# Optimization experiments

Hardware: AMD Instinct MI355X
Metric: run time of the kernel (lower is better)

Reference implementation:

```python
import jax, jax.numpy as jnp
import numpy as np

H = 256        # hidden_size
MAX_LEN = 200  # position table has MAX_LEN+1 rows
B = 4096       # number of sessions


def setup_inputs() -> dict:
    rng = np.random.RandomState(0)
    # ragged session lengths in [10, 100)
    seq_len = rng.randint(10, 100, size=B).astype(np.int64)
    T = int(seq_len.sum())
    # reverse positions: len-1, ..., 1, 0 per session (as the torch code uses)
    reverse_pos = np.concatenate([np.arange(l - 1, -1, -1) for l in seq_len]).astype(np.int64)

    key = jax.random.key(0)
    ks = jax.random.split(key, 8)
    def lin(k, fin, fout):
        # torch Linear init ~ U(-1/sqrt(fin), 1/sqrt(fin)); store as [fin, fout]
        lim = 1.0 / np.sqrt(fin)
        kw, kb = jax.random.split(k)
        W = jax.random.uniform(kw, (fin, fout), jnp.float32, -lim, lim)
        b = jax.random.uniform(kb, (fout,), jnp.float32, -lim, lim)
        return W, b

    hidden = jax.random.normal(ks[0], (T, H), jnp.float32)
    pos_table = jax.random.normal(ks[1], (MAX_LEN + 1, H), jnp.float32)
    W_pos, b_pos = lin(ks[2], 2 * H, H)   # W_pos_inter
    W1, b1 = lin(ks[3], H, H)             # W_1_inter
    W2, b2 = lin(ks[4], H, H)             # W_2_inter
    qw, qb = lin(ks[5], H, 1)             # q_inter

    return {
        "hidden": hidden,
        "pos_table": pos_table,
        "W_pos": W_pos, "b_pos": b_pos,
        "W1": W1, "b1": b1,
        "W2": W2, "b2": b2,
        "qw": qw, "qb": qb,
        "seq_len": jnp.asarray(seq_len),
        "reverse_pos": jnp.asarray(reverse_pos),
    }


def reference(hidden, pos_table, W_pos, b_pos, W1, b1, W2, b2, qw, qb, seq_len, reverse_pos):
    T = hidden.shape[0]
    nb = seq_len.shape[0]
    # segment id per token (sessions are contiguous)
    seg = jnp.repeat(jnp.arange(nb), seq_len, total_repeat_length=T)  # [T]
    # per-session mean, gathered back per token (v_mean_repeat_concat)
    sess_mean = jax.ops.segment_sum(hidden, seg, num_segments=nb)
    sess_mean = sess_mean / seq_len[:, None].astype(hidden.dtype)
    v_mean = sess_mean[seg]                                           # [T, H]
    # position-augmented hidden: tanh(W_pos_inter([hidden; pos_emb]))
    pos_emb = pos_table[reverse_pos]                                  # [T, H]
    pos_hidden = jnp.tanh(jnp.concatenate([hidden, pos_emb], -1) @ W_pos + b_pos)
    # alpha = q_inter(sigmoid(W_1_inter(v_mean) + W_2_inter(pos_hidden)))
    gate = jax.nn.sigmoid(v_mean @ W1 + b1 + pos_hidden @ W2 + b2)
    alpha = gate @ qw + qb                                            # [T, 1]
    # per-session weighted sum of hidden
    h_s = jax.ops.segment_sum(alpha * hidden, seg, num_segments=nb)   # [B, H]
    return h_s
```

## Files before the change

kernel.cpp:

```cpp
#include <hip/hip_runtime.h>
#include <hip/hip_bf16.h>
#include <stdint.h>

#define HD 256
#define BM 64
#define APAD 8
#define ASTRIDE (HD + APAD)

typedef __bf16 bf16x8 __attribute__((ext_vector_type(8)));
typedef float f32x4 __attribute__((ext_vector_type(4)));
typedef unsigned short ushort8v __attribute__((ext_vector_type(8)));
typedef unsigned short us4 __attribute__((ext_vector_type(4)));

__device__ __forceinline__ unsigned short f2bf(float f) {
    unsigned int x = __float_as_uint(f);
    unsigned int r = (x + 0x7FFFu + ((x >> 16) & 1u)) >> 16;
    return (unsigned short)r;
}

__global__ void scan_kernel(const int* __restrict__ seq_len, int* __restrict__ offsets, int B) {
    __shared__ int sums[256];
    int tid = threadIdx.x;
    int per = (B + 255) / 256;
    int b0 = tid * per;
    int local[32];
    int tot = 0;
    for (int i = 0; i < per && i < 32; ++i) {
        int b = b0 + i;
        int v = (b < B) ? seq_len[b] : 0;
        local[i] = tot;
        tot += v;
    }
    sums[tid] = tot;
    __syncthreads();
    for (int off = 1; off < 256; off <<= 1) {
        int v = (tid >= off) ? sums[tid - off] : 0;
        __syncthreads();
        sums[tid] += v;
        __syncthreads();
    }
    int start = sums[tid] - tot;
    for (int i = 0; i < per && i < 32; ++i) {
        int b = b0 + i;
        if (b < B) offsets[b] = start + local[i];
    }
    if (tid == 255) offsets[B] = sums[255];
}

__global__ void mean_kernel(const float* __restrict__ hidden, const int* __restrict__ offsets,
                            unsigned short* __restrict__ mean_bf, unsigned short* __restrict__ hb,
                            int* __restrict__ seg) {
    int b = blockIdx.x;
    int s = offsets[b], e = offsets[b + 1];
    int tid = threadIdx.x;
    for (int t = s + tid; t < e; t += 256) seg[t] = b;
    int g = tid >> 6, c = tid & 63;
    float4 acc = {0.f, 0.f, 0.f, 0.f};
    for (int t = s + g; t < e; t += 4) {
        const float4 v = *reinterpret_cast<const float4*>(hidden + (size_t)t * HD + c * 4);
        acc.x += v.x; acc.y += v.y; acc.z += v.z; acc.w += v.w;
        if (hb) {
            us4 pk;
            pk[0] = f2bf(v.x); pk[1] = f2bf(v.y); pk[2] = f2bf(v.z); pk[3] = f2bf(v.w);
            *reinterpret_cast<us4*>(hb + (size_t)t * HD + c * 4) = pk;
        }
    }
    __shared__ float4 part[4][64];
    part[g][c] = acc;
    __syncthreads();
    if (g == 0) {
        float4 a0 = part[0][c], a1 = part[1][c], a2 = part[2][c], a3 = part[3][c];
        float inv = 1.0f / (float)(e - s);
        us4 pk;
        pk[0] = f2bf((a0.x + a1.x + a2.x + a3.x) * inv);
        pk[1] = f2bf((a0.y + a1.y + a2.y + a3.y) * inv);
        pk[2] = f2bf((a0.z + a1.z + a2.z + a3.z) * inv);
        pk[3] = f2bf((a0.w + a1.w + a2.w + a3.w) * inv);
        *reinterpret_cast<us4*>(mean_bf + (size_t)b * HD + c * 4) = pk;
    }
}

__global__ void transpose_kernel(const float* __restrict__ Wp, const float* __restrict__ W1,
                                 const float* __restrict__ W2,
                                 unsigned short* __restrict__ WphT, unsigned short* __restrict__ WpbT,
                                 unsigned short* __restrict__ W1T, unsigned short* __restrict__ W2T) {
    int n = blockIdx.x;
    int k = threadIdx.x;
    WphT[n * HD + k] = f2bf(Wp[k * HD + n]);
    WpbT[n * HD + k] = f2bf(Wp[(HD + k) * HD + n]);
    W1T[n * HD + k]  = f2bf(W1[k * HD + n]);
    W2T[n * HD + k]  = f2bf(W2[k * HD + n]);
}

__global__ __launch_bounds__(256) void small_gemm_kernel(
    const unsigned short* __restrict__ mean_bf, int Mu, int nbu,
    const float* __restrict__ pos_table, int Mp,
    const unsigned short* __restrict__ W1T, const unsigned short* __restrict__ WpbT,
    const float* __restrict__ b1, const float* __restrict__ b2, const float* __restrict__ bp,
    float* __restrict__ u, float* __restrict__ P2) {
    __shared__ __align__(16) unsigned short As[16][ASTRIDE];
    int tid = threadIdx.x;
    bool isU = (int)blockIdx.x < nbu;
    int m0 = isU ? blockIdx.x * 16 : (blockIdx.x - nbu) * 16;
    int M  = isU ? Mu : Mp;
    const unsigned short* BT = isU ? W1T : WpbT;
    float* out = isU ? u : P2;

    {
        int row = tid >> 4;
        int colg = (tid & 15) * 16;
        int m = m0 + row;
        if (isU) {
            ushort8v v0 = {0,0,0,0,0,0,0,0}, v1 = {0,0,0,0,0,0,0,0};
            if (m < M) {
                v0 = *reinterpret_cast<const ushort8v*>(mean_bf + (size_t)m * HD + colg);
                v1 = *reinterpret_cast<const ushort8v*>(mean_bf + (size_t)m * HD + colg + 8);
            }
            *reinterpret_cast<ushort8v*>(&As[row][colg])     = v0;
            *reinterpret_cast<ushort8v*>(&As[row][colg + 8]) = v1;
        } else {
            float4 f[4] = {{0,0,0,0},{0,0,0,0},{0,0,0,0},{0,0,0,0}};
            if (m < M) {
                const float4* p = reinterpret_cast<const float4*>(pos_table + (size_t)m * HD + colg);
                f[0] = p[0]; f[1] = p[1]; f[2] = p[2]; f[3] = p[3];
            }
            ushort8v v0, v1;
            v0[0]=f2bf(f[0].x); v0[1]=f2bf(f[0].y); v0[2]=f2bf(f[0].z); v0[3]=f2bf(f[0].w);
            v0[4]=f2bf(f[1].x); v0[5]=f2bf(f[1].y); v0[6]=f2bf(f[1].z); v0[7]=f2bf(f[1].w);
            v1[0]=f2bf(f[2].x); v1[1]=f2bf(f[2].y); v1[2]=f2bf(f[2].z); v1[3]=f2bf(f[2].w);
            v1[4]=f2bf(f[3].x); v1[5]=f2bf(f[3].y); v1[6]=f2bf(f[3].z); v1[7]=f2bf(f[3].w);
            *reinterpret_cast<ushort8v*>(&As[row][colg])     = v0;
            *reinterpret_cast<ushort8v*>(&As[row][colg + 8]) = v1;
        }
    }
    __syncthreads();

    int wave = tid >> 6, lane = tid & 63, quad = lane >> 4, cc = lane & 15;
    int nb = wave * 64;
    f32x4 acc4[4];
    for (int i = 0; i < 4; ++i) acc4[i] = (f32x4){0.f, 0.f, 0.f, 0.f};

    bf16x8 wfp[4];
    for (int nf = 0; nf < 4; ++nf)
        wfp[nf] = *reinterpret_cast<const bf16x8*>(BT + (size_t)(nb + nf * 16 + cc) * HD + quad * 8);
    for (int kc8 = 0; kc8 < 8; ++kc8) {
        int kc = kc8 * 32;
        bf16x8 wfc[4];
        for (int nf = 0; nf < 4; ++nf) wfc[nf] = wfp[nf];
        if (kc8 < 7)
            for (int nf = 0; nf < 4; ++nf)
                wfp[nf] = *reinterpret_cast<const bf16x8*>(BT + (size_t)(nb + nf * 16 + cc) * HD + kc + 32 + quad * 8);
        bf16x8 af = *reinterpret_cast<const bf16x8*>(&As[cc][kc + quad * 8]);
        for (int nf = 0; nf < 4; ++nf)
            acc4[nf] = __builtin_amdgcn_mfma_f32_16x16x32_bf16(af, wfc[nf], acc4[nf], 0, 0, 0);
    }
    for (int nf = 0; nf < 4; ++nf)
        for (int r = 0; r < 4; ++r) {
            int row = m0 + quad * 4 + r;
            int col = nb + nf * 16 + cc;
            if (row < M) {
                float bias = isU ? (b1[col] + b2[col]) : bp[col];
                out[(size_t)row * HD + col] = acc4[nf][r] + bias;
            }
        }
}

__global__ __launch_bounds__(256, 3) void main_kernel(
    const float* __restrict__ hidden, const unsigned short* __restrict__ hb, int T,
    const unsigned short* __restrict__ WphT,
    const unsigned short* __restrict__ W2T,
    const float* __restrict__ P2,
    const float* __restrict__ u,
    const float* __restrict__ qw, const float* __restrict__ qb,
    const int* __restrict__ rp, const int* __restrict__ seg,
    float* __restrict__ alpha) {
    __shared__ __align__(16) unsigned short Ah[BM][ASTRIDE];
    __shared__ int rp_s[BM];
    __shared__ int seg_s[BM];
    __shared__ float alpha_s[BM];

    int tid = threadIdx.x;
    int t0 = blockIdx.x * BM;
    int wave = tid >> 6, lane = tid & 63, quad = lane >> 4, cc = lane & 15;
    int mb = wave * 64;

    bf16x8 afp[4];
    for (int mf = 0; mf < 4; ++mf)
        afp[mf] = *reinterpret_cast<const bf16x8*>(WphT + (size_t)(mb + mf * 16 + cc) * HD + quad * 8);

    {
        int row = tid >> 2;
        int t = t0 + row;
        if (hb) {
            for (int i = 0; i < 8; ++i) {
                int cg = (tid & 3) * 8 + 32 * i;
                ushort8v v = {0,0,0,0,0,0,0,0};
                if (t < T) v = *reinterpret_cast<const ushort8v*>(hb + (size_t)t * HD + cg);
                *reinterpret_cast<ushort8v*>(&Ah[row][cg]) = v;
            }
        } else {
            for (int i = 0; i < 8; ++i) {
                int cg = (tid & 3) * 8 + 32 * i;
                float4 f0 = {0,0,0,0}, f1 = {0,0,0,0};
                if (t < T) {
                    const float4* p = reinterpret_cast<const float4*>(hidden + (size_t)t * HD + cg);
                    f0 = p[0]; f1 = p[1];
                }
                ushort8v pk;
                pk[0] = f2bf(f0.x); pk[1] = f2bf(f0.y); pk[2] = f2bf(f0.z); pk[3] = f2bf(f0.w);
                pk[4] = f2bf(f1.x); pk[5] = f2bf(f1.y); pk[6] = f2bf(f1.z); pk[7] = f2bf(f1.w);
                *reinterpret_cast<ushort8v*>(&Ah[row][cg]) = pk;
            }
        }
    }
    if (tid < BM) {
        int t = t0 + tid;
        rp_s[tid]  = (t < T) ? rp[t] : 0;
        seg_s[tid] = (t < T) ? seg[t] : 0;
        alpha_s[tid] = qb[0];
    }
    __syncthreads();

    f32x4 acc[4][4];
    for (int i = 0; i < 4; ++i) for (int j = 0; j < 4; ++j) acc[i][j] = (f32x4){0.f, 0.f, 0.f, 0.f};

    for (int kc8 = 0; kc8 < 8; ++kc8) {
        int kc = kc8 * 32;
        bf16x8 afc[4];
        for (int mf = 0; mf < 4; ++mf) afc[mf] = afp[mf];
        if (kc8 < 7)
            for (int mf = 0; mf < 4; ++mf)
                afp[mf] = *reinterpret_cast<const bf16x8*>(WphT + (size_t)(mb + mf * 16 + cc) * HD + kc + 32 + quad * 8);
        bf16x8 bfr[4];
        for (int nf = 0; nf < 4; ++nf)
            bfr[nf] = *reinterpret_cast<const bf16x8*>(&Ah[nf * 16 + cc][kc + quad * 8]);
        for (int mf = 0; mf < 4; ++mf)
            for (int nf = 0; nf < 4; ++nf)
                acc[mf][nf] = __builtin_amdgcn_mfma_f32_16x16x32_bf16(afc[mf], bfr[nf], acc[mf][nf], 0, 0, 0);
    }
    __syncthreads();

    bf16x8 wfp[4];
    for (int nf = 0; nf < 4; ++nf)
        wfp[nf] = *reinterpret_cast<const bf16x8*>(W2T + (size_t)(mb + nf * 16 + cc) * HD + quad * 8);

    for (int mf = 0; mf < 4; ++mf)
        for (int nf = 0; nf < 4; ++nf) {
            int token = nf * 16 + cc;
            int h0 = mb + mf * 16 + quad * 4;
            const float4 p2v = *reinterpret_cast<const float4*>(P2 + (size_t)rp_s[token] * HD + h0);
            us4 pk;
            {
                float v0 = acc[mf][nf][0] + p2v.x;
                float v1 = acc[mf][nf][1] + p2v.y;
                float v2 = acc[mf][nf][2] + p2v.z;
                float v3 = acc[mf][nf][3] + p2v.w;
                float e0 = __expf(2.f * v0), e1 = __expf(2.f * v1);
                float e2 = __expf(2.f * v2), e3 = __expf(2.f * v3);
                pk[0] = f2bf(1.f - 2.f / (e0 + 1.f));
                pk[1] = f2bf(1.f - 2.f / (e1 + 1.f));
                pk[2] = f2bf(1.f - 2.f / (e2 + 1.f));
                pk[3] = f2bf(1.f - 2.f / (e3 + 1.f));
            }
            *reinterpret_cast<us4*>(&Ah[token][h0]) = pk;
            acc[mf][nf] = (f32x4){0.f, 0.f, 0.f, 0.f};
        }
    __syncthreads();

    for (int kc8 = 0; kc8 < 8; ++kc8) {
        int kc = kc8 * 32;
        bf16x8 wfc[4];
        for (int nf = 0; nf < 4; ++nf) wfc[nf] = wfp[nf];
        if (kc8 < 7)
            for (int nf = 0; nf < 4; ++nf)
                wfp[nf] = *reinterpret_cast<const bf16x8*>(W2T + (size_t)(mb + nf * 16 + cc) * HD + kc + 32 + quad * 8);
        for (int mf = 0; mf < 4; ++mf) {
            bf16x8 af = *reinterpret_cast<const bf16x8*>(&Ah[mf * 16 + cc][kc + quad * 8]);
            for (int nf = 0; nf < 4; ++nf)
                acc[mf][nf] = __builtin_amdgcn_mfma_f32_16x16x32_bf16(af, wfc[nf], acc[mf][nf], 0, 0, 0);
        }
    }

    float qwv[4];
    for (int nf = 0; nf < 4; ++nf) qwv[nf] = qw[mb + nf * 16 + cc];
    for (int mf = 0; mf < 4; ++mf)
        for (int r = 0; r < 4; ++r) {
            int token = mf * 16 + quad * 4 + r;
            const float* urow = u + (size_t)seg_s[token] * HD;
            float s = 0.f;
            for (int nf = 0; nf < 4; ++nf) {
                float g = acc[mf][nf][r] + urow[mb + nf * 16 + cc];
                g = 1.0f / (1.0f + __expf(-g));
                s += g * qwv[nf];
            }
            s += __shfl_xor(s, 1);
            s += __shfl_xor(s, 2);
            s += __shfl_xor(s, 4);
            s += __shfl_xor(s, 8);
            if (cc == 0) atomicAdd(&alpha_s[token], s);
        }
    __syncthreads();
    if (tid < BM) {
        int t = t0 + tid;
        if (t < T) alpha[t] = alpha_s[tid];
    }
}

__global__ void hs_kernel(const float* __restrict__ hidden, const unsigned short* __restrict__ hb,
                          const float* __restrict__ alpha,
                          const int* __restrict__ offsets, float* __restrict__ out) {
    int b = blockIdx.x;
    int s = offsets[b], e = offsets[b + 1];
    int tid = threadIdx.x;
    __shared__ float al[256];
    for (int i = tid; i < e - s; i += 256) al[i] = alpha[s + i];
    __syncthreads();
    int g = tid >> 6, c = tid & 63;
    float4 acc = {0.f, 0.f, 0.f, 0.f};
    if (hb) {
        for (int t = s + g; t < e; t += 4) {
            float a = al[t - s];
            us4 v = *reinterpret_cast<const us4*>(hb + (size_t)t * HD + c * 4);
            acc.x += a * __uint_as_float(((unsigned)v[0]) << 16);
            acc.y += a * __uint_as_float(((unsigned)v[1]) << 16);
            acc.z += a * __uint_as_float(((unsigned)v[2]) << 16);
            acc.w += a * __uint_as_float(((unsigned)v[3]) << 16);
        }
    } else {
        for (int t = s + g; t < e; t += 4) {
            float a = al[t - s];
            const float4 v = *reinterpret_cast<const float4*>(hidden + (size_t)t * HD + c * 4);
            acc.x += a * v.x; acc.y += a * v.y; acc.z += a * v.z; acc.w += a * v.w;
        }
    }
    __shared__ float4 part[4][64];
    part[g][c] = acc;
    __syncthreads();
    if (g == 0) {
        float4 a0 = part[0][c], a1 = part[1][c], a2 = part[2][c], a3 = part[3][c];
        float4 m;
        m.x = a0.x + a1.x + a2.x + a3.x;
        m.y = a0.y + a1.y + a2.y + a3.y;
        m.z = a0.z + a1.z + a2.z + a3.z;
        m.w = a0.w + a1.w + a2.w + a3.w;
        *reinterpret_cast<float4*>(out + (size_t)b * HD + c * 4) = m;
    }
}

extern "C" void kernel_launch(void* const* d_in, const int* in_sizes, int n_in,
                              void* d_out, int out_size, void* d_ws, size_t ws_size,
                              hipStream_t stream) {
    (void)n_in; (void)out_size;
    const float* hidden    = (const float*)d_in[0];
    const float* pos_table = (const float*)d_in[1];
    const float* W_pos     = (const float*)d_in[2];
    const float* b_pos     = (const float*)d_in[3];
    const float* W1        = (const float*)d_in[4];
    const float* b1        = (const float*)d_in[5];
    const float* W2        = (const float*)d_in[6];
    const float* b2        = (const float*)d_in[7];
    const float* qw        = (const float*)d_in[8];
    const float* qb        = (const float*)d_in[9];
    const int* seq_len     = (const int*)d_in[10];
    const int* reverse_pos = (const int*)d_in[11];

    int T  = in_sizes[0] / HD;
    int B  = in_sizes[10];
    int NP = in_sizes[1] / HD;

    char* ws = (char*)d_ws;
    char* ws_end = ws + ws_size;
    auto carve = [&](size_t bytes) -> char* {
        char* p = ws;
        ws += (bytes + 255) & ~(size_t)255;
        return p;
    };
    int* offsets          = (int*)carve((size_t)(B + 1) * sizeof(int));
    int* seg              = (int*)carve((size_t)T * sizeof(int));
    unsigned short* meanb = (unsigned short*)carve((size_t)B * HD * 2);
    float* u              = (float*)carve((size_t)B * HD * sizeof(float));
    float* P2             = (float*)carve((size_t)NP * HD * sizeof(float));
    unsigned short* WphT  = (unsigned short*)carve((size_t)HD * HD * 2);
    unsigned short* WpbT  = (unsigned short*)carve((size_t)HD * HD * 2);
    unsigned short* W1T   = (unsigned short*)carve((size_t)HD * HD * 2);
    unsigned short* W2T   = (unsigned short*)carve((size_t)HD * HD * 2);
    float* alpha          = (float*)carve((size_t)T * sizeof(float));
    unsigned short* hb    = nullptr;
    if ((size_t)(ws_end - ws) >= (size_t)T * HD * 2 + 256)
        hb = (unsigned short*)carve((size_t)T * HD * 2);

    int nbu = (B + 15) / 16;
    int nbp = (NP + 15) / 16;

    scan_kernel<<<1, 256, 0, stream>>>(seq_len, offsets, B);
    transpose_kernel<<<HD, HD, 0, stream>>>(W_pos, W1, W2, WphT, WpbT, W1T, W2T);
    mean_kernel<<<B, 256, 0, stream>>>(hidden, offsets, meanb, hb, seg);
    small_gemm_kernel<<<nbu + nbp, 256, 0, stream>>>(meanb, B, nbu, pos_table, NP,
                                                     W1T, WpbT, b1, b2, b_pos, u, P2);
    main_kernel<<<(T + BM - 1) / BM, 256, 0, stream>>>(hidden, hb, T, WphT, W2T, P2, u, qw, qb,
                                                       reverse_pos, seg, alpha);
    hs_kernel<<<B, 256, 0, stream>>>(hidden, hb, alpha, offsets, (float*)d_out);
}
```

Baseline: 575.5 us.

## Fuse scan with weight transpose, fold mean GEMV into mean kernel, deepen weight prefetch

```diff
diff --git a/kernel.cpp b/kernel.cpp
--- a/kernel.cpp
+++ b/kernel.cpp
@@ -17,110 +17,115 @@
     unsigned int r = (x + 0x7FFFu + ((x >> 16) & 1u)) >> 16;
     return (unsigned short)r;
 }
-
-__global__ void scan_kernel(const int* __restrict__ seq_len, int* __restrict__ offsets, int B) {
-    __shared__ int sums[256];
+__device__ __forceinline__ float bf2f(unsigned short h) {
+    return __uint_as_float(((unsigned)h) << 16);
+}
+
+__global__ void setup_kernel(const int* __restrict__ seq_len, int* __restrict__ offsets, int B,
+                             const float* __restrict__ Wp, const float* __restrict__ W1,
+                             const float* __restrict__ W2,
+                             unsigned short* __restrict__ WphT, unsigned short* __restrict__ WpbT,
+                             unsigned short* __restrict__ W1b, unsigned short* __restrict__ W2T) {
     int tid = threadIdx.x;
-    int per = (B + 255) / 256;
-    int b0 = tid * per;
-    int local[32];
-    int tot = 0;
-    for (int i = 0; i < per && i < 32; ++i) {
-        int b = b0 + i;
-        int v = (b < B) ? seq_len[b] : 0;
-        local[i] = tot;
-        tot += v;
-    }
-    sums[tid] = tot;
-    __syncthreads();
-    for (int off = 1; off < 256; off <<= 1) {
-        int v = (tid >= off) ? sums[tid - off] : 0;
+    if (blockIdx.x == 0) {
+        __shared__ int sums[256];
+        int per = (B + 255) / 256;
+        int b0 = tid * per;
+        int local[32];
+        int tot = 0;
+        for (int i = 0; i < per && i < 32; ++i) {
+            int b = b0 + i;
+            int v = (b < B) ? seq_len[b] : 0;
+            local[i] = tot;
+            tot += v;
+        }
+        sums[tid] = tot;
         __syncthreads();
-        sums[tid] += v;
-        __syncthreads();
-    }
-    int start = sums[tid] - tot;
-    for (int i = 0; i < per && i < 32; ++i) {
-        int b = b0 + i;
-        if (b < B) offsets[b] = start + local[i];
-    }
-    if (tid == 255) offsets[B] = sums[255];
-}
-
-__global__ void mean_kernel(const float* __restrict__ hidden, const int* __restrict__ offsets,
-                            unsigned short* __restrict__ mean_bf, unsigned short* __restrict__ hb,
-                            int* __restrict__ seg) {
-    int b = blockIdx.x;
-    int s = offsets[b], e = offsets[b + 1];
-    int tid = threadIdx.x;
-    for (int t = s + tid; t < e; t += 256) seg[t] = b;
-    int g = tid >> 6, c = tid & 63;
-    float4 acc = {0.f, 0.f, 0.f, 0.f};
-    for (int t = s + g; t < e; t += 4) {
-        const float4 v = *reinterpret_cast<const float4*>(hidden + (size_t)t * HD + c * 4);
-        acc.x += v.x; acc.y += v.y; acc.z += v.z; acc.w += v.w;
-        if (hb) {
-            us4 pk;
-            pk[0] = f2bf(v.x); pk[1] = f2bf(v.y); pk[2] = f2bf(v.z); pk[3] = f2bf(v.w);
-            *reinterpret_cast<us4*>(hb + (size_t)t * HD + c * 4) = pk;
-        }
-    }
+        for (int off = 1; off < 256; off <<= 1) {
+            int v = (tid >= off) ? sums[tid - off] : 0;
+            __syncthreads();
+            sums[tid] += v;
+            __syncthreads();
+        }
+        int start = sums[tid] - tot;
+        for (int i = 0; i < per && i < 32; ++i) {
+            int b = b0 + i;
+            if (b < B) offsets[b] = start + local[i];
+        }
+        if (tid == 255) offsets[B] = sums[255];
+    } else {
+        int n = blockIdx.x - 1;
+        int k = tid;
+        WphT[n * HD + k] = f2bf(Wp[k * HD + n]);
+        WpbT[n * HD + k] = f2bf(Wp[(HD + k) * HD + n]);
+        W2T[n * HD + k]  = f2bf(W2[k * HD + n]);
+        W1b[n * HD + k]  = f2bf(W1[n * HD + k]);
+    }
+}
+
+__global__ __launch_bounds__(256) void mean_u_p2_kernel(
+    const float* __restrict__ hidden, const int* __restrict__ offsets, int B,
+    unsigned short* __restrict__ hb, int* __restrict__ seg,
+    const unsigned short* __restrict__ W1b,
+    const float* __restrict__ b1, const float* __restrict__ b2,
+    float* __restrict__ u,
+    const float* __restrict__ pos_table, int Mp,
+    const unsigned short* __restrict__ WpbT, const float* __restrict__ bp,
+    float* __restrict__ P2) {
     __shared__ float4 part[4][64];
-    part[g][c] = acc;
-    __syncthreads();
-    if (g == 0) {
-        float4 a0 = part[0][c], a1 = part[1][c], a2 = part[2][c], a3 = part[3][c];
-        float inv = 1.0f / (float)(e - s);
-        us4 pk;
-        pk[0] = f2bf((a0.x + a1.x + a2.x + a3.x) * inv);
-        pk[1] = f2bf((a0.y + a1.y + a2.y + a3.y) * inv);
-        pk[2] = f2bf((a0.z + a1.z + a2.z + a3.z) * inv);
-        pk[3] = f2bf((a0.w + a1.w + a2.w + a3.w) * inv);
-        *reinterpret_cast<us4*>(mean_bf + (size_t)b * HD + c * 4) = pk;
-    }
-}
-
-__global__ void transpose_kernel(const float* __restrict__ Wp, const float* __restrict__ W1,
-                                 const float* __restrict__ W2,
-                                 unsigned short* __restrict__ WphT, unsigned short* __restrict__ WpbT,
-                                 unsigned short* __restrict__ W1T, unsigned short* __restrict__ W2T) {
-    int n = blockIdx.x;
-    int k = threadIdx.x;
-    WphT[n * HD + k] = f2bf(Wp[k * HD + n]);
-    WpbT[n * HD + k] = f2bf(Wp[(HD + k) * HD + n]);
-    W1T[n * HD + k]  = f2bf(W1[k * HD + n]);
-    W2T[n * HD + k]  = f2bf(W2[k * HD + n]);
-}
-
-__global__ __launch_bounds__(256) void small_gemm_kernel(
-    const unsigned short* __restrict__ mean_bf, int Mu, int nbu,
-    const float* __restrict__ pos_table, int Mp,
-    const unsigned short* __restrict__ W1T, const unsigned short* __restrict__ WpbT,
-    const float* __restrict__ b1, const float* __restrict__ b2, const float* __restrict__ bp,
-    float* __restrict__ u, float* __restrict__ P2) {
+    __shared__ float m_s[HD];
     __shared__ __align__(16) unsigned short As[16][ASTRIDE];
     int tid = threadIdx.x;
-    bool isU = (int)blockIdx.x < nbu;
-    int m0 = isU ? blockIdx.x * 16 : (blockIdx.x - nbu) * 16;
-    int M  = isU ? Mu : Mp;
-    const unsigned short* BT = isU ? W1T : WpbT;
-    float* out = isU ? u : P2;
-
-    {
-        int row = tid >> 4;
-        int colg = (tid & 15) * 16;
-        int m = m0 + row;
-        if (isU) {
-            ushort8v v0 = {0,0,0,0,0,0,0,0}, v1 = {0,0,0,0,0,0,0,0};
-            if (m < M) {
-                v0 = *reinterpret_cast<const ushort8v*>(mean_bf + (size_t)m * HD + colg);
-                v1 = *reinterpret_cast<const ushort8v*>(mean_bf + (size_t)m * HD + colg + 8);
-            }
-            *reinterpret_cast<ushort8v*>(&As[row][colg])     = v0;
-            *reinterpret_cast<ushort8v*>(&As[row][colg + 8]) = v1;
-        } else {
+
+    if ((int)blockIdx.x < B) {
+        int b = blockIdx.x;
+        int s = offsets[b], e = offsets[b + 1];
+        for (int t = s + tid; t < e; t += 256) seg[t] = b;
+        int g = tid >> 6, c = tid & 63;
+        float4 acc = {0.f, 0.f, 0.f, 0.f};
+        for (int t = s + g; t < e; t += 4) {
+            const float4 v = *reinterpret_cast<const float4*>(hidden + (size_t)t * HD + c * 4);
+            acc.x += v.x; acc.y += v.y; acc.z += v.z; acc.w += v.w;
+            if (hb) {
+                us4 pk;
+                pk[0] = f2bf(v.x); pk[1] = f2bf(v.y); pk[2] = f2bf(v.z); pk[3] = f2bf(v.w);
+                *reinterpret_cast<us4*>(hb + (size_t)t * HD + c * 4) = pk;
+            }
+        }
+        part[g][c] = acc;
+        __syncthreads();
+        if (g == 0) {
+            float4 a0 = part[0][c], a1 = part[1][c], a2 = part[2][c], a3 = part[3][c];
+            float inv = 1.0f / (float)(e - s);
+            m_s[c * 4 + 0] = (a0.x + a1.x + a2.x + a3.x) * inv;
+            m_s[c * 4 + 1] = (a0.y + a1.y + a2.y + a3.y) * inv;
+            m_s[c * 4 + 2] = (a0.z + a1.z + a2.z + a3.z) * inv;
+            m_s[c * 4 + 3] = (a0.w + a1.w + a2.w + a3.w) * inv;
+        }
+        __syncthreads();
+        int n = tid;
+        float sacc = 0.f;
+        #pragma unroll 4
+        for (int k = 0; k < HD; k += 8) {
+            float p0 = m_s[k + 0] * bf2f(W1b[(size_t)(k + 0) * HD + n]);
+            float p1 = m_s[k + 1] * bf2f(W1b[(size_t)(k + 1) * HD + n]);
+            float p2_ = m_s[k + 2] * bf2f(W1b[(size_t)(k + 2) * HD + n]);
+            float p3 = m_s[k + 3] * bf2f(W1b[(size_t)(k + 3) * HD + n]);
+            float p4 = m_s[k + 4] * bf2f(W1b[(size_t)(k + 4) * HD + n]);
+            float p5 = m_s[k + 5] * bf2f(W1b[(size_t)(k + 5) * HD + n]);
+            float p6 = m_s[k + 6] * bf2f(W1b[(size_t)(k + 6) * HD + n]);
+            float p7 = m_s[k + 7] * bf2f(W1b[(size_t)(k + 7) * HD + n]);
+            sacc += ((p0 + p1) + (p2_ + p3)) + ((p4 + p5) + (p6 + p7));
+        }
+        u[(size_t)b * HD + n] = sacc + b1[n] + b2[n];
+    } else {
+        int m0 = ((int)blockIdx.x - B) * 16;
+        {
+            int row = tid >> 4;
+            int colg = (tid & 15) * 16;
+            int m = m0 + row;
             float4 f[4] = {{0,0,0,0},{0,0,0,0},{0,0,0,0},{0,0,0,0}};
-            if (m < M) {
+            if (m < Mp) {
                 const float4* p = reinterpret_cast<const float4*>(pos_table + (size_t)m * HD + colg);
                 f[0] = p[0]; f[1] = p[1]; f[2] = p[2]; f[3] = p[3];
             }
@@ -132,37 +137,33 @@
             *reinterpret_cast<ushort8v*>(&As[row][colg])     = v0;
             *reinterpret_cast<ushort8v*>(&As[row][colg + 8]) = v1;
         }
-    }
-    __syncthreads();
-
-    int wave = tid >> 6, lane = tid & 63, quad = lane >> 4, cc = lane & 15;
-    int nb = wave * 64;
-    f32x4 acc4[4];
-    for (int i = 0; i < 4; ++i) acc4[i] = (f32x4){0.f, 0.f, 0.f, 0.f};
-
-    bf16x8 wfp[4];
-    for (int nf = 0; nf < 4; ++nf)
-        wfp[nf] = *reinterpret_cast<const bf16x8*>(BT + (size_t)(nb + nf * 16 + cc) * HD + quad * 8);
-    for (int kc8 = 0; kc8 < 8; ++kc8) {
-        int kc = kc8 * 32;
-        bf16x8 wfc[4];
-        for (int nf = 0; nf < 4; ++nf) wfc[nf] = wfp[nf];
-        if (kc8 < 7)
+        __syncthreads();
+        int wave = tid >> 6, lane = tid & 63, quad = lane >> 4, cc = lane & 15;
+        int nb = wave * 64;
+        f32x4 acc4[4];
+        for (int i = 0; i < 4; ++i) acc4[i] = (f32x4){0.f, 0.f, 0.f, 0.f};
+        bf16x8 wfp[4];
+        for (int nf = 0; nf < 4; ++nf)
+            wfp[nf] = *reinterpret_cast<const bf16x8*>(WpbT + (size_t)(nb + nf * 16 + cc) * HD + quad * 8);
+        for (int kc8 = 0; kc8 < 8; ++kc8) {
+            int kc = kc8 * 32;
+            bf16x8 wfc[4];
+            for (int nf = 0; nf < 4; ++nf) wfc[nf] = wfp[nf];
+            if (kc8 < 7)
+                for (int nf = 0; nf < 4; ++nf)
+                    wfp[nf] = *reinterpret_cast<const bf16x8*>(WpbT + (size_t)(nb + nf * 16 + cc) * HD + kc + 32 + quad * 8);
+            bf16x8 af = *reinterpret_cast<const bf16x8*>(&As[cc][kc + quad * 8]);
             for (int nf = 0; nf < 4; ++nf)
-                wfp[nf] = *reinterpret_cast<const bf16x8*>(BT + (size_t)(nb + nf * 16 + cc) * HD + kc + 32 + quad * 8);
-        bf16x8 af = *reinterpret_cast<const bf16x8*>(&As[cc][kc + quad * 8]);
+                acc4[nf] = __builtin_amdgcn_mfma_f32_16x16x32_bf16(af, wfc[nf], acc4[nf], 0, 0, 0);
+        }
         for (int nf = 0; nf < 4; ++nf)
-            acc4[nf] = __builtin_amdgcn_mfma_f32_16x16x32_bf16(af, wfc[nf], acc4[nf], 0, 0, 0);
-    }
-    for (int nf = 0; nf < 4; ++nf)
-        for (int r = 0; r < 4; ++r) {
-            int row = m0 + quad * 4 + r;
-            int col = nb + nf * 16 + cc;
-            if (row < M) {
-                float bias = isU ? (b1[col] + b2[col]) : bp[col];
-                out[(size_t)row * HD + col] = acc4[nf][r] + bias;
-            }
-        }
+            for (int r = 0; r < 4; ++r) {
+                int row = m0 + quad * 4 + r;
+                int col = nb + nf * 16 + cc;
+                if (row < Mp)
+                    P2[(size_t)row * HD + col] = acc4[nf][r] + bp[col];
+            }
+    }
 }
 
 __global__ __launch_bounds__(256, 3) void main_kernel(
@@ -184,9 +185,10 @@
     int wave = tid >> 6, lane = tid & 63, quad = lane >> 4, cc = lane & 15;
     int mb = wave * 64;
 
-    bf16x8 afp[4];
-    for (int mf = 0; mf < 4; ++mf)
-        afp[mf] = *reinterpret_cast<const bf16x8*>(WphT + (size_t)(mb + mf * 16 + cc) * HD + quad * 8);
+    bf16x8 afp[4][4];
+    for (int s = 0; s < 4; ++s)
+        for (int mf = 0; mf < 4; ++mf)
+            afp[s][mf] = *reinterpret_cast<const bf16x8*>(WphT + (size_t)(mb + mf * 16 + cc) * HD + s * 32 + quad * 8);
 
     {
         int row = tid >> 2;
@@ -226,11 +228,12 @@
 
     for (int kc8 = 0; kc8 < 8; ++kc8) {
         int kc = kc8 * 32;
+        int slot = kc8 & 3;
         bf16x8 afc[4];
-        for (int mf = 0; mf < 4; ++mf) afc[mf] = afp[mf];
-        if (kc8 < 7)
+        for (int mf = 0; mf < 4; ++mf) afc[mf] = afp[slot][mf];
+        if (kc8 < 4)
             for (int mf = 0; mf < 4; ++mf)
-                afp[mf] = *reinterpret_cast<const bf16x8*>(WphT + (size_t)(mb + mf * 16 + cc) * HD + kc + 32 + quad * 8);
+                afp[slot][mf] = *reinterpret_cast<const bf16x8*>(WphT + (size_t)(mb + mf * 16 + cc) * HD + kc + 128 + quad * 8);
         bf16x8 bfr[4];
         for (int nf = 0; nf < 4; ++nf)
             bfr[nf] = *reinterpret_cast<const bf16x8*>(&Ah[nf * 16 + cc][kc + quad * 8]);
@@ -238,11 +241,13 @@
             for (int nf = 0; nf < 4; ++nf)
                 acc[mf][nf] = __builtin_amdgcn_mfma_f32_16x16x32_bf16(afc[mf], bfr[nf], acc[mf][nf], 0, 0, 0);
     }
-    __syncthreads();
-
-    bf16x8 wfp[4];
-    for (int nf = 0; nf < 4; ++nf)
-        wfp[nf] = *reinterpret_cast<const bf16x8*>(W2T + (size_t)(mb + nf * 16 + cc) * HD + quad * 8);
+
+    bf16x8 wfp[4][4];
+    for (int s = 0; s < 4; ++s)
+        for (int nf = 0; nf < 4; ++nf)
+            wfp[s][nf] = *reinterpret_cast<const bf16x8*>(W2T + (size_t)(mb + nf * 16 + cc) * HD + s * 32 + quad * 8);
+
+    __syncthreads();
 
     for (int mf = 0; mf < 4; ++mf)
         for (int nf = 0; nf < 4; ++nf) {
@@ -269,11 +274,12 @@
 
     for (int kc8 = 0; kc8 < 8; ++kc8) {
         int kc = kc8 * 32;
+        int slot = kc8 & 3;
         bf16x8 wfc[4];
-        for (int nf = 0; nf < 4; ++nf) wfc[nf] = wfp[nf];
-        if (kc8 < 7)
+        for (int nf = 0; nf < 4; ++nf) wfc[nf] = wfp[slot][nf];
+        if (kc8 < 4)
             for (int nf = 0; nf < 4; ++nf)
-                wfp[nf] = *reinterpret_cast<const bf16x8*>(W2T + (size_t)(mb + nf * 16 + cc) * HD + kc + 32 + quad * 8);
+                wfp[slot][nf] = *reinterpret_cast<const bf16x8*>(W2T + (size_t)(mb + nf * 16 + cc) * HD + kc + 128 + quad * 8);
         for (int mf = 0; mf < 4; ++mf) {
             bf16x8 af = *reinterpret_cast<const bf16x8*>(&Ah[mf * 16 + cc][kc + quad * 8]);
             for (int nf = 0; nf < 4; ++nf)
@@ -321,10 +327,10 @@
         for (int t = s + g; t < e; t += 4) {
             float a = al[t - s];
             us4 v = *reinterpret_cast<const us4*>(hb + (size_t)t * HD + c * 4);
-            acc.x += a * __uint_as_float(((unsigned)v[0]) << 16);
-            acc.y += a * __uint_as_float(((unsigned)v[1]) << 16);
-            acc.z += a * __uint_as_float(((unsigned)v[2]) << 16);
-            acc.w += a * __uint_as_float(((unsigned)v[3]) << 16);
+            acc.x += a * bf2f(v[0]);
+            acc.y += a * bf2f(v[1]);
+            acc.z += a * bf2f(v[2]);
+            acc.w += a * bf2f(v[3]);
         }
     } else {
         for (int t = s + g; t < e; t += 4) {
@@ -377,26 +383,24 @@
     };
     int* offsets          = (int*)carve((size_t)(B + 1) * sizeof(int));
     int* seg              = (int*)carve((size_t)T * sizeof(int));
-    unsigned short* meanb = (unsigned short*)carve((size_t)B * HD * 2);
     float* u              = (float*)carve((size_t)B * HD * sizeof(float));
     float* P2             = (float*)carve((size_t)NP * HD * sizeof(float));
     unsigned short* WphT  = (unsigned short*)carve((size_t)HD * HD * 2);
     unsigned short* WpbT  = (unsigned short*)carve((size_t)HD * HD * 2);
-    unsigned short* W1T   = (unsigned short*)carve((size_t)HD * HD * 2);
+    unsigned short* W1b   = (unsigned short*)carve((size_t)HD * HD * 2);
     unsigned short* W2T   = (unsigned short*)carve((size_t)HD * HD * 2);
     float* alpha          = (float*)carve((size_t)T * sizeof(float));
     unsigned short* hb    = nullptr;
     if ((size_t)(ws_end - ws) >= (size_t)T * HD * 2 + 256)
         hb = (unsigned short*)carve((size_t)T * HD * 2);
 
-    int nbu = (B + 15) / 16;
     int nbp = (NP + 15) / 16;
 
-    scan_kernel<<<1, 256, 0, stream>>>(seq_len, offsets, B);
-    transpose_kernel<<<HD, HD, 0, stream>>>(W_pos, W1, W2, WphT, WpbT, W1T, W2T);
-    mean_kernel<<<B, 256, 0, stream>>>(hidden, offsets, meanb, hb, seg);
-    small_gemm_kernel<<<nbu + nbp, 256, 0, stream>>>(meanb, B, nbu, pos_table, NP,
-                                                     W1T, WpbT, b1, b2, b_pos, u, P2);
+    setup_kernel<<<HD + 1, 256, 0, stream>>>(seq_len, offsets, B, W_pos, W1, W2,
+                                             WphT, WpbT, W1b, W2T);
+    mean_u_p2_kernel<<<B + nbp, 256, 0, stream>>>(hidden, offsets, B, hb, seg,
+                                                  W1b, b1, b2, u,
+                                                  pos_table, NP, WpbT, b_pos, P2);
     main_kernel<<<(T + BM - 1) / BM, 256, 0, stream>>>(hidden, hb, T, WphT, W2T, P2, u, qw, qb,
                                                        reverse_pos, seg, alpha);
     hs_kernel<<<B, 256, 0, stream>>>(hidden, hb, alpha, offsets, (float*)d_out);
```

Result: slower. 603.3 us (+4.8%).
